# Kernel tuning notes

Hardware: AMD Instinct MI355X
Metric: run time of the kernel (lower is better)

## Reference

```python
import jax, jax.numpy as jnp
import numpy as np

D = 512
H = 4 * D
EPS = 1e-5

def layernorm(x, g, b):
    mu = jnp.mean(x, axis=-1, keepdims=True)
    var = jnp.mean((x - mu) ** 2, axis=-1, keepdims=True)
    return (x - mu) * jax.lax.rsqrt(var + EPS) * g + b

def setup_inputs() -> dict:
    key = jax.random.key(0)
    ks = jax.random.split(key, 16)
    s = 0.02
    inp = {
        "x": jax.random.normal(ks[0], (16, 2048, D), dtype=jnp.float32),
        "wq": jax.random.normal(ks[1], (D, D), dtype=jnp.float32) * s,
        "bq": jnp.zeros((D,), jnp.float32),
        "wk": jax.random.normal(ks[2], (D, D), dtype=jnp.float32) * s,
        "bk": jnp.zeros((D,), jnp.float32),
        "wv": jax.random.normal(ks[3], (D, D), dtype=jnp.float32) * s,
        "bv": jnp.zeros((D,), jnp.float32),
        "wp": jax.random.normal(ks[4], (D, D), dtype=jnp.float32) * s,
        "bp": jnp.zeros((D,), jnp.float32),
        "w1": jax.random.normal(ks[5], (D, H), dtype=jnp.float32) * s,
        "b1": jnp.zeros((H,), jnp.float32),
        "w2": jax.random.normal(ks[6], (H, D), dtype=jnp.float32) * s,
        "b2": jnp.zeros((D,), jnp.float32),
        "g1": jnp.ones((D,), jnp.float32),
        "be1": jnp.zeros((D,), jnp.float32),
        "g2": jnp.ones((D,), jnp.float32),
        "be2": jnp.zeros((D,), jnp.float32),
    }
    return inp

def reference(x, wq, bq, wk, bk, wv, bv, wp, bp, w1, b1, w2, b2, g1, be1, g2, be2):
    temperature = jnp.sqrt(jnp.asarray(D, x.dtype))
    q = x @ wq + bq                      # [B,N,D]
    k = x @ wk + bk
    v = x @ wv + bv
    energy = jnp.einsum('bnd,bmd->bnm', q / temperature, k)   # [B,N,N]
    attn = jax.nn.softmax(energy, axis=-1)
    out = jnp.einsum('bnm,bmd->bnd', attn, v)
    att = out @ wp + bp
    x = layernorm(x + att, g1, be1)
    h = jax.nn.gelu(x @ w1 + b1, approximate=False)
    ff = h @ w2 + b2
    x = layernorm(x + ff, g2, be2)
    return x
```

## Files before the change

### kernel.cpp

```cpp
#include <hip/hip_runtime.h>
#include <cmath>

typedef __bf16 bf16_t;
typedef __bf16 bf16x8 __attribute__((ext_vector_type(8)));
typedef __bf16 bf16x4 __attribute__((ext_vector_type(4)));
typedef float f32x4 __attribute__((ext_vector_type(4)));

#define DEV_INLINE __device__ __forceinline__

DEV_INLINE void gload_lds16(const void* g, void* l) {
  __builtin_amdgcn_global_load_lds(
      (const __attribute__((address_space(1))) void*)g,
      (__attribute__((address_space(3))) void*)l, 16, 0, 0);
}

DEV_INLINE float gelu_f(float v) {
  const float u = v * (0.7978845608f + 0.0356774081f * v * v);
  const float e = __expf(2.f * u);
  const float th = 1.f - 2.f / (e + 1.f);
  return 0.5f * v * (1.f + th);
}

template<int EPI, bool HAS_BIAS>
__global__ __launch_bounds__(256, 2)
void gemm_n256(const bf16_t* __restrict__ A, const bf16_t* __restrict__ B,
               const float* __restrict__ bias, bf16_t* __restrict__ C,
               int M, int N, int K, int lda, int ldb, int ldc,
               long sA, long sB, long sC, float scale)
{
  __shared__ alignas(16) bf16_t As[3][4096];
  __shared__ alignas(16) bf16_t Bs[3][8192];
  const int b = blockIdx.z;
  A += (long)b * sA;
  B += (long)b * sB;
  const int t  = threadIdx.x;
  const int l  = t & 63;
  const int w  = t >> 6;
  const int wr   = (w >> 1) * 64;
  const int wcol = (w & 1) * 128;

  const int gx  = gridDim.x;
  const int nwg = gx * gridDim.y;
  int id = blockIdx.y * gx + blockIdx.x;
  id = (id & 7) * (nwg >> 3) + (id >> 3);
  const int m0 = (id / gx) * 128;
  const int n0 = (id % gx) * 256;

  const int r0 = t >> 2;
  const int wb = (t & 3) * 16;
  const int cbs = wb ^ (((r0 >> 1) & 3) << 4);
  const bf16_t* gA0 = A + (long)(m0 + r0) * lda + (cbs >> 1);
  const bf16_t* gA1 = A + (long)(m0 + r0 + 64) * lda + (cbs >> 1);
  const bf16_t* gB0 = B + (long)(n0 + r0) * ldb + (cbs >> 1);

#define STAGE6(kt, q) do {                                       \
    const long ko_ = (long)(kt) * 32;                            \
    gload_lds16(gA0 + ko_, &As[q][t * 8]);                       \
    gload_lds16(gA1 + ko_, &As[q][2048 + t * 8]);                \
    gload_lds16(gB0 + ko_,                   &Bs[q][t * 8]);     \
    gload_lds16(gB0 +  64 * (long)ldb + ko_, &Bs[q][2048 + t * 8]); \
    gload_lds16(gB0 + 128 * (long)ldb + ko_, &Bs[q][4096 + t * 8]); \
    gload_lds16(gB0 + 192 * (long)ldb + ko_, &Bs[q][6144 + t * 8]); \
  } while (0)

  const int fr  = l & 15;
  const int kkb = (l >> 4) * 16;
  int offA[4], offB[8];
#pragma unroll
  for (int mi = 0; mi < 4; mi++) {
    const int row = wr + mi * 16 + fr;
    offA[mi] = row * 32 + ((kkb ^ (((row >> 1) & 3) << 4)) >> 1);
  }
#pragma unroll
  for (int ni = 0; ni < 8; ni++) {
    const int row = wcol + ni * 16 + fr;
    offB[ni] = row * 32 + ((kkb ^ (((row >> 1) & 3) << 4)) >> 1);
  }

  f32x4 acc[4][8] = {};

  const int NT = K >> 5;
  STAGE6(0, 0);
  STAGE6(1, 1);

  int q = 0;
  for (int kt = 0; kt < NT; ++kt) {
    if (kt < NT - 1) asm volatile("s_waitcnt vmcnt(6)" ::: "memory");
    else             asm volatile("s_waitcnt vmcnt(0)" ::: "memory");
    __builtin_amdgcn_sched_barrier(0);
    __builtin_amdgcn_s_barrier();

    if (kt + 2 < NT) {
      int qs = q + 2; if (qs >= 3) qs -= 3;
      STAGE6(kt + 2, qs);
    }

    bf16x8 af[4];
#pragma unroll
    for (int mi = 0; mi < 4; mi++)
      af[mi] = *(const bf16x8*)&As[q][offA[mi]];
#pragma unroll
    for (int nh = 0; nh < 2; nh++) {
      bf16x8 bf4[4];
#pragma unroll
      for (int nj = 0; nj < 4; nj++)
        bf4[nj] = *(const bf16x8*)&Bs[q][offB[nh * 4 + nj]];
#pragma unroll
      for (int mi = 0; mi < 4; mi++)
#pragma unroll
        for (int nj = 0; nj < 4; nj++)
          acc[mi][nh * 4 + nj] = __builtin_amdgcn_mfma_f32_16x16x32_bf16(
              bf4[nj], af[mi], acc[mi][nh * 4 + nj], 0, 0, 0);
    }

    if (++q == 3) q = 0;
  }
#undef STAGE6

  const long cb = (long)b * sC;
  const int cq = (l >> 4) * 4;
#pragma unroll
  for (int mi = 0; mi < 4; mi++) {
    const int row = m0 + wr + mi * 16 + fr;
    bf16_t* crow = C + cb + (long)row * ldc;
#pragma unroll
    for (int ni = 0; ni < 8; ni++) {
      const int c0 = n0 + wcol + ni * 16 + cq;
      float4 b4 = {0.f, 0.f, 0.f, 0.f};
      if constexpr (HAS_BIAS) b4 = *(const float4*)&bias[c0];
      float vv[4] = { acc[mi][ni][0] + b4.x, acc[mi][ni][1] + b4.y,
                      acc[mi][ni][2] + b4.z, acc[mi][ni][3] + b4.w };
      if constexpr (EPI == 2) {
#pragma unroll
        for (int r = 0; r < 4; r++) vv[r] *= scale;
      }
      if constexpr (EPI == 3) {
#pragma unroll
        for (int r = 0; r < 4; r++) vv[r] = gelu_f(vv[r]);
      }
      if constexpr (EPI == 6) {
#pragma unroll
        for (int r = 0; r < 4; r++) vv[r] = __expf(vv[r] * scale);
      }
      bf16x4 pk = { (bf16_t)vv[0], (bf16_t)vv[1],
                    (bf16_t)vv[2], (bf16_t)vv[3] };
      *(bf16x4*)(crow + c0) = pk;
    }
  }
}

template<int EPI, bool HAS_BIAS>
__global__ __launch_bounds__(256, 2)
void gemm_bt(const bf16_t* __restrict__ A, const bf16_t* __restrict__ B,
             const float* __restrict__ bias, void* __restrict__ C,
             bf16_t* __restrict__ vTaux,
             int M, int N, int K, int lda, int ldb, int ldc,
             long sA, long sB, long sC, float scale)
{
  constexpr bool SWAP = (EPI == 1 || EPI == 2 || EPI == 3 || EPI == 4);
  __shared__ alignas(16) bf16_t lds[3][2][4096];
  const int b = blockIdx.z;
  A += (long)b * sA;
  B += (long)b * sB;
  const int t  = threadIdx.x;
  const int l  = t & 63;
  const int w  = t >> 6;
  const int wr = (w >> 1) * 64;
  const int wc = (w & 1) * 64;

  const int gx  = gridDim.x;
  const int nwg = gx * gridDim.y;
  int id = blockIdx.y * gx + blockIdx.x;
  id = (id & 7) * (nwg >> 3) + (id >> 3);
  const int m0 = (id / gx) * 128;
  const int n0 = (id % gx) * 128;

  const int r0 = t >> 2;
  const int r1 = r0 + 64;
  const int wb = (t & 3) * 16;
  const int cbs0 = wb ^ (((r0 >> 1) & 3) << 4);
  const int cbs1 = wb ^ (((r1 >> 1) & 3) << 4);
  const bf16_t* gA0 = A + (long)(m0 + r0) * lda + (cbs0 >> 1);
  const bf16_t* gA1 = A + (long)(m0 + r1) * lda + (cbs1 >> 1);
  const bf16_t* gB0 = B + (long)(n0 + r0) * ldb + (cbs0 >> 1);
  const bf16_t* gB1 = B + (long)(n0 + r1) * ldb + (cbs1 >> 1);

#define STAGE(kt, q) do {                                   \
    const long kofs_ = (long)(kt) * 32;                     \
    gload_lds16(gA0 + kofs_, &lds[q][0][t * 8]);            \
    gload_lds16(gA1 + kofs_, &lds[q][0][2048 + t * 8]);     \
    gload_lds16(gB0 + kofs_, &lds[q][1][t * 8]);            \
    gload_lds16(gB1 + kofs_, &lds[q][1][2048 + t * 8]);     \
  } while (0)

  const int fr  = l & 15;
  const int kkb = (l >> 4) * 16;
  int offA[4], offB[4];
#pragma unroll
  for (int mi = 0; mi < 4; mi++) {
    const int row = wr + mi * 16 + fr;
    offA[mi] = row * 32 + ((kkb ^ (((row >> 1) & 3) << 4)) >> 1);
  }
#pragma unroll
  for (int ni = 0; ni < 4; ni++) {
    const int row = wc + ni * 16 + fr;
    offB[ni] = row * 32 + ((kkb ^ (((row >> 1) & 3) << 4)) >> 1);
  }

  f32x4 acc[4][4] = {};

  const int NT = K >> 5;
  STAGE(0, 0);
  STAGE(1, 1);

  int q = 0;
  for (int kt = 0; kt < NT; ++kt) {
    if (kt < NT - 1) asm volatile("s_waitcnt vmcnt(4)" ::: "memory");
    else             asm volatile("s_waitcnt vmcnt(0)" ::: "memory");
    __builtin_amdgcn_sched_barrier(0);
    __builtin_amdgcn_s_barrier();

    if (kt + 2 < NT) {
      int qs = q + 2; if (qs >= 3) qs -= 3;
      STAGE(kt + 2, qs);
    }

    bf16x8 af[4], bfr[4];
#pragma unroll
    for (int mi = 0; mi < 4; mi++)
      af[mi] = *(const bf16x8*)&lds[q][0][offA[mi]];
#pragma unroll
    for (int ni = 0; ni < 4; ni++)
      bfr[ni] = *(const bf16x8*)&lds[q][1][offB[ni]];
#pragma unroll
    for (int mi = 0; mi < 4; mi++)
#pragma unroll
      for (int ni = 0; ni < 4; ni++) {
        if constexpr (SWAP)
          acc[mi][ni] = __builtin_amdgcn_mfma_f32_16x16x32_bf16(
              bfr[ni], af[mi], acc[mi][ni], 0, 0, 0);
        else
          acc[mi][ni] = __builtin_amdgcn_mfma_f32_16x16x32_bf16(
              af[mi], bfr[ni], acc[mi][ni], 0, 0, 0);
      }

    if (++q == 3) q = 0;
  }
#undef STAGE

  const long cb = (long)b * sC;

  if constexpr (SWAP) {
    const int cq = (l >> 4) * 4;
#pragma unroll
    for (int mi = 0; mi < 4; mi++) {
      const int row = m0 + wr + mi * 16 + fr;
      bf16_t* crow = (bf16_t*)C + cb + (long)row * ldc;
      float rs = 1.f;
      if constexpr (EPI == 4) rs = bias[(long)b * 2048 + row];
#pragma unroll
      for (int ni = 0; ni < 4; ni++) {
        const int c0 = n0 + wc + ni * 16 + cq;
        float4 b4 = {0.f, 0.f, 0.f, 0.f};
        if constexpr (HAS_BIAS) b4 = *(const float4*)&bias[c0];
        float vv[4] = { acc[mi][ni][0] + b4.x, acc[mi][ni][1] + b4.y,
                        acc[mi][ni][2] + b4.z, acc[mi][ni][3] + b4.w };
        if constexpr (EPI == 2) {
#pragma unroll
          for (int r = 0; r < 4; r++) vv[r] *= scale;
        }
        if constexpr (EPI == 3) {
#pragma unroll
          for (int r = 0; r < 4; r++) vv[r] = gelu_f(vv[r]);
        }
        if constexpr (EPI == 4) {
#pragma unroll
          for (int r = 0; r < 4; r++) vv[r] *= rs;
        }
        bf16x4 pk = { (bf16_t)vv[0], (bf16_t)vv[1],
                      (bf16_t)vv[2], (bf16_t)vv[3] };
        *(bf16x4*)(crow + c0) = pk;
      }
    }
    return;
  }

  const int rbase = m0 + wr + (l >> 4) * 4;
#pragma unroll
  for (int mi = 0; mi < 4; mi++) {
    const int row0 = rbase + mi * 16;
#pragma unroll
    for (int ni = 0; ni < 4; ni++) {
      const int c = n0 + wc + ni * 16 + fr;
      float bias_v = 0.f;
      if constexpr (HAS_BIAS) bias_v = bias[c];
      float vals[4];
#pragma unroll
      for (int r = 0; r < 4; r++) vals[r] = acc[mi][ni][r] + bias_v;
      if (c < 1024) {
#pragma unroll
        for (int r = 0; r < 4; r++)
          ((bf16_t*)C)[(long)(row0 + r) * ldc + c] = (bf16_t)vals[r];
      } else {
        const int bb = row0 >> 11;
        const int n  = row0 & 2047;
        bf16x4 pk = { (bf16_t)vals[0], (bf16_t)vals[1],
                      (bf16_t)vals[2], (bf16_t)vals[3] };
        *(bf16x4*)&vTaux[(long)bb * (512 * 2048) + (long)(c - 1024) * 2048 + n] = pk;
      }
    }
  }
}

__global__ __launch_bounds__(256)
void transpose_cast(const float* __restrict__ in, bf16_t* __restrict__ out,
                    int R, int Cc)
{
  __shared__ float tile[32][33];
  const int c0 = blockIdx.x * 32;
  const int r0 = blockIdx.y * 32;
  const int tx = threadIdx.x & 31;
  const int ty = threadIdx.x >> 5;
#pragma unroll
  for (int i = 0; i < 32; i += 8)
    tile[ty + i][tx] = in[(long)(r0 + ty + i) * Cc + (c0 + tx)];
  __syncthreads();
#pragma unroll
  for (int i = 0; i < 32; i += 8)
    out[(long)(c0 + ty + i) * R + (r0 + tx)] = (bf16_t)tile[tx][ty + i];
}

__global__ __launch_bounds__(256)
void cast_to_bf16(const float* __restrict__ in, bf16_t* __restrict__ out, long n)
{
  const long i = ((long)blockIdx.x * 256 + threadIdx.x) * 4;
  if (i >= n) return;
  const float4 v = *(const float4*)&in[i];
  bf16x4 o = { (bf16_t)v.x, (bf16_t)v.y, (bf16_t)v.z, (bf16_t)v.w };
  *(bf16x4*)&out[i] = o;
}

__global__ __launch_bounds__(256)
void concat_bias(const float* __restrict__ a, const float* __restrict__ b,
                 const float* __restrict__ c, float* __restrict__ o)
{
  const int i = blockIdx.x * 256 + threadIdx.x;
  if (i < 512) o[i] = a[i];
  else if (i < 1024) o[i] = b[i - 512];
  else if (i < 1536) o[i] = c[i - 1024];
}

__global__ __launch_bounds__(256)
void rowsum2048(const bf16_t* __restrict__ P, float* __restrict__ inv_s)
{
  const long row = blockIdx.x;
  const bf16_t* p = P + row * 2048;
  const int t = threadIdx.x;
  bf16x8 xv = *(const bf16x8*)&p[t * 8];
  float s = 0.f;
#pragma unroll
  for (int j = 0; j < 8; j++) s += (float)xv[j];
  for (int o = 32; o; o >>= 1) s += __shfl_xor(s, o);
  __shared__ float reds[4];
  if ((t & 63) == 0) reds[t >> 6] = s;
  __syncthreads();
  if (t == 0)
    inv_s[row] = 1.f / (reds[0] + reds[1] + reds[2] + reds[3]);
}

template<bool EMIT_F32, bool EMIT_BF16>
__global__ __launch_bounds__(128)
void add_ln(const bf16_t* __restrict__ xa, const bf16_t* __restrict__ xadd,
            const float* __restrict__ g, const float* __restrict__ be,
            float* __restrict__ y, bf16_t* __restrict__ yb)
{
  const long row = blockIdx.x;
  const int c = threadIdx.x * 4;
  bf16x4 a = *(const bf16x4*)&xa[row * 512 + c];
  bf16x4 d = *(const bf16x4*)&xadd[row * 512 + c];
  float vv[4];
#pragma unroll
  for (int j = 0; j < 4; j++) vv[j] = (float)a[j] + (float)d[j];
  float s = 0.f, s2 = 0.f;
#pragma unroll
  for (int j = 0; j < 4; j++) { s += vv[j]; s2 += vv[j] * vv[j]; }
  for (int o = 32; o; o >>= 1) { s += __shfl_xor(s, o); s2 += __shfl_xor(s2, o); }
  __shared__ float r0[2], r1[2];
  const int w = threadIdx.x >> 6;
  if ((threadIdx.x & 63) == 0) { r0[w] = s; r1[w] = s2; }
  __syncthreads();
  s = r0[0] + r0[1]; s2 = r1[0] + r1[1];
  const float mu = s * (1.f / 512.f);
  const float var = s2 * (1.f / 512.f) - mu * mu;
  const float rstd = rsqrtf(var + 1e-5f);
  const float4 gg = *(const float4*)&g[c];
  const float4 bev = *(const float4*)&be[c];
  float o0 = (vv[0] - mu) * rstd * gg.x + bev.x;
  float o1 = (vv[1] - mu) * rstd * gg.y + bev.y;
  float o2 = (vv[2] - mu) * rstd * gg.z + bev.z;
  float o3 = (vv[3] - mu) * rstd * gg.w + bev.w;
  if constexpr (EMIT_F32) {
    float4 yo = { o0, o1, o2, o3 };
    *(float4*)&y[row * 512 + c] = yo;
  }
  if constexpr (EMIT_BF16) {
    bf16x4 ob = { (bf16_t)o0, (bf16_t)o1, (bf16_t)o2, (bf16_t)o3 };
    *(bf16x4*)&yb[row * 512 + c] = ob;
  }
}

extern "C" void kernel_launch(void* const* d_in, const int* in_sizes, int n_in,
                              void* d_out, int out_size, void* d_ws, size_t ws_size,
                              hipStream_t stream)
{
  const float* x   = (const float*)d_in[0];
  const float* wq  = (const float*)d_in[1];
  const float* bq  = (const float*)d_in[2];
  const float* wk  = (const float*)d_in[3];
  const float* bk  = (const float*)d_in[4];
  const float* wv  = (const float*)d_in[5];
  const float* bv  = (const float*)d_in[6];
  const float* wp  = (const float*)d_in[7];
  const float* bp  = (const float*)d_in[8];
  const float* w1  = (const float*)d_in[9];
  const float* b1  = (const float*)d_in[10];
  const float* w2  = (const float*)d_in[11];
  const float* b2  = (const float*)d_in[12];
  const float* g1  = (const float*)d_in[13];
  const float* be1 = (const float*)d_in[14];
  const float* g2  = (const float*)d_in[15];
  const float* be2 = (const float*)d_in[16];

  const long S = 16L * 2048 * 512;
  const long Mi = 1L << 20;

  const size_t NEED = (size_t)232 * Mi;
  if (ws_size < NEED) return;

  char* wsp = (char*)d_ws;
  bf16_t* wqkvT = (bf16_t*)(wsp + 0);
  bf16_t* wpT   = wqkvT + 1536L * 512;
  bf16_t* w1T   = wpT + 512L * 512;
  bf16_t* w2T   = w1T + 2048L * 512;
  float*  bqkv  = (float*)(w2T + 512L * 2048);
  float*  inv_s = (float*)(wsp + 7 * Mi);
  bf16_t* xb    = (bf16_t*)(wsp +   8 * Mi);
  bf16_t* qkb   = (bf16_t*)(wsp +  40 * Mi);
  bf16_t* vT    = (bf16_t*)(wsp + 104 * Mi);
  bf16_t* E     = (bf16_t*)(wsp + 136 * Mi);
  bf16_t* ob    = (bf16_t*)(wsp + 200 * Mi);
  bf16_t* x1b   = qkb;
  bf16_t* h     = (bf16_t*)(wsp + 72 * Mi);
  bf16_t* projb = E;
  bf16_t* ffb   = xb;

  cast_to_bf16<<<dim3((unsigned)(S / 4 / 256)), 256, 0, stream>>>(x, xb, S);

  transpose_cast<<<dim3(16, 16), 256, 0, stream>>>(wq, wqkvT,               512, 512);
  transpose_cast<<<dim3(16, 16), 256, 0, stream>>>(wk, wqkvT + 512L * 512,  512, 512);
  transpose_cast<<<dim3(16, 16), 256, 0, stream>>>(wv, wqkvT + 1024L * 512, 512, 512);
  transpose_cast<<<dim3(16, 16), 256, 0, stream>>>(wp, wpT, 512, 512);
  transpose_cast<<<dim3(64, 16), 256, 0, stream>>>(w1, w1T, 512, 2048);
  transpose_cast<<<dim3(16, 64), 256, 0, stream>>>(w2, w2T, 2048, 512);
  concat_bias<<<dim3(6), 256, 0, stream>>>(bq, bk, bv, bqkv);

  gemm_bt<5, true><<<dim3(12, 256, 1), 256, 0, stream>>>(
      xb, wqkvT, bqkv, qkb, vT, 32768, 1536, 512, 512, 512, 1024, 0, 0, 0, 0.f);

  for (int cgrp = 0; cgrp < 2; cgrp++) {
    const long qoff = (long)cgrp * 8 * 2048 * 1024;
    gemm_n256<6, false><<<dim3(8, 16, 8), 256, 0, stream>>>(
        qkb + qoff, qkb + qoff + 512, nullptr, E,
        2048, 2048, 512, 1024, 1024, 2048,
        2048L * 1024, 2048L * 1024, 2048L * 2048, 0.04419417382f);
    rowsum2048<<<dim3(16384), 256, 0, stream>>>(E, inv_s);
    gemm_bt<4, false><<<dim3(4, 16, 8), 256, 0, stream>>>(
        E, vT + (long)cgrp * 8 * 512 * 2048, inv_s,
        ob + (long)cgrp * 8 * 2048 * 512, nullptr,
        2048, 512, 2048, 2048, 2048, 512,
        2048L * 2048, 512L * 2048, 2048L * 512, 0.f);
  }

  gemm_n256<1, true><<<dim3(2, 256, 1), 256, 0, stream>>>(
      ob, wpT, bp, projb,
      32768, 512, 512, 512, 512, 512, 0, 0, 0, 0.f);

  add_ln<false, true><<<dim3(32768), 128, 0, stream>>>(
      xb, projb, g1, be1, nullptr, x1b);

  gemm_bt<3, true><<<dim3(16, 256, 1), 256, 0, stream>>>(
      x1b, w1T, b1, h, nullptr, 32768, 2048, 512, 512, 512, 2048, 0, 0, 0, 0.f);

  gemm_n256<1, true><<<dim3(2, 256, 1), 256, 0, stream>>>(
      h, w2T, b2, ffb,
      32768, 512, 2048, 2048, 2048, 512, 0, 0, 0, 0.f);

  add_ln<true, false><<<dim3(32768), 128, 0, stream>>>(
      x1b, ffb, g2, be2, (float*)d_out, nullptr);
}
```

Baseline: 581.5 us.

## Fuse softmax row-sum into P·V GEMM via ones-vector MFMA

Removes the separate rowsum2048 kernel and computes each row's softmax denominator inside the P·V GEMM. It issues one extra MFMA per row tile against a ones vector, reusing the A fragments already in registers. This saves a full extra read of the 2048x2048 probability matrix per batch group and one launch. The cost is four extra MFMAs per k-step and more accumulator registers. The sum is taken from the same bf16 values used in the product, and lane/row mapping must match for correctness.

```diff
diff --git a/kernel.cpp b/kernel.cpp
--- a/kernel.cpp
+++ b/kernel.cpp
@@ -208,6 +208,12 @@
   }
 
   f32x4 acc[4][4] = {};
+  f32x4 sacc[4] = {};
+  bf16x8 ones;
+  if constexpr (EPI == 4) {
+#pragma unroll
+    for (int j = 0; j < 8; j++) ones[j] = (bf16_t)1.f;
+  }
 
   const int NT = K >> 5;
   STAGE(0, 0);
@@ -243,6 +249,12 @@
           acc[mi][ni] = __builtin_amdgcn_mfma_f32_16x16x32_bf16(
               af[mi], bfr[ni], acc[mi][ni], 0, 0, 0);
       }
+    if constexpr (EPI == 4) {
+#pragma unroll
+      for (int mi = 0; mi < 4; mi++)
+        sacc[mi] = __builtin_amdgcn_mfma_f32_16x16x32_bf16(
+            ones, af[mi], sacc[mi], 0, 0, 0);
+    }
 
     if (++q == 3) q = 0;
   }
@@ -257,7 +269,7 @@
       const int row = m0 + wr + mi * 16 + fr;
       bf16_t* crow = (bf16_t*)C + cb + (long)row * ldc;
       float rs = 1.f;
-      if constexpr (EPI == 4) rs = bias[(long)b * 2048 + row];
+      if constexpr (EPI == 4) rs = 1.f / sacc[mi][0];
 #pragma unroll
       for (int ni = 0; ni < 4; ni++) {
         const int c0 = n0 + wc + ni * 16 + cq;
@@ -348,24 +360,6 @@
   if (i < 512) o[i] = a[i];
   else if (i < 1024) o[i] = b[i - 512];
   else if (i < 1536) o[i] = c[i - 1024];
-}
-
-__global__ __launch_bounds__(256)
-void rowsum2048(const bf16_t* __restrict__ P, float* __restrict__ inv_s)
-{
-  const long row = blockIdx.x;
-  const bf16_t* p = P + row * 2048;
-  const int t = threadIdx.x;
-  bf16x8 xv = *(const bf16x8*)&p[t * 8];
-  float s = 0.f;
-#pragma unroll
-  for (int j = 0; j < 8; j++) s += (float)xv[j];
-  for (int o = 32; o; o >>= 1) s += __shfl_xor(s, o);
-  __shared__ float reds[4];
-  if ((t & 63) == 0) reds[t >> 6] = s;
-  __syncthreads();
-  if (t == 0)
-    inv_s[row] = 1.f / (reds[0] + reds[1] + reds[2] + reds[3]);
 }
 
 template<bool EMIT_F32, bool EMIT_BF16>
@@ -443,7 +437,6 @@
   bf16_t* w1T   = wpT + 512L * 512;
   bf16_t* w2T   = w1T + 2048L * 512;
   float*  bqkv  = (float*)(w2T + 512L * 2048);
-  float*  inv_s = (float*)(wsp + 7 * Mi);
   bf16_t* xb    = (bf16_t*)(wsp +   8 * Mi);
   bf16_t* qkb   = (bf16_t*)(wsp +  40 * Mi);
   bf16_t* vT    = (bf16_t*)(wsp + 104 * Mi);
@@ -473,9 +466,8 @@
         qkb + qoff, qkb + qoff + 512, nullptr, E,
         2048, 2048, 512, 1024, 1024, 2048,
         2048L * 1024, 2048L * 1024, 2048L * 2048, 0.04419417382f);
-    rowsum2048<<<dim3(16384), 256, 0, stream>>>(E, inv_s);
     gemm_bt<4, false><<<dim3(4, 16, 8), 256, 0, stream>>>(
-        E, vT + (long)cgrp * 8 * 512 * 2048, inv_s,
+        E, vT + (long)cgrp * 8 * 512 * 2048, nullptr,
         ob + (long)cgrp * 8 * 2048 * 512, nullptr,
         2048, 512, 2048, 2048, 2048, 512,
         2048L * 2048, 512L * 2048, 2048L * 512, 0.f);
```

Measured after the change: 562.4 us, median of 3. -3.3%, faster.
